# Kernel tuning notes

Measured on AMD Instinct MI355X. Metric: run time of the kernel, lower is better.

Reference implementation:

```python
import jax, jax.numpy as jnp
import numpy as np
import math

B, L, D = 8, 2048, 256


def setup_inputs() -> dict:
    key = jax.random.key(0)
    ks = jax.random.split(key, 8)
    return {
        "query": jax.random.normal(ks[0], (B, L, D), dtype=jnp.float32),
        "key": jax.random.normal(ks[1], (B, L, D), dtype=jnp.float32),
        "value": jax.random.normal(ks[2], (B, L, D), dtype=jnp.float32),
        "mask": jax.random.randint(ks[3], (B, L), 0, 2, dtype=jnp.int32),
        "Wq_w": jax.random.normal(ks[4], (D, D), dtype=jnp.float32) * 0.05,
        "Wq_b": jax.random.normal(ks[5], (D,), dtype=jnp.float32) * 0.05,
        "Wk_w": jax.random.normal(ks[6], (D, D), dtype=jnp.float32) * 0.05,
        "Wk_b": jax.random.normal(ks[7], (D,), dtype=jnp.float32) * 0.05,
    }


def reference(query, key, value, mask, Wq_w, Wq_b, Wk_w, Wk_b):
    d = query.shape[-1]
    q = query @ Wq_w.T + Wq_b            # [B, Lq, D]
    k = key @ Wk_w.T + Wk_b              # [B, Lk, D]
    scores = jnp.einsum("bqd,bkd->bqk", q, k) / math.sqrt(d)  # [B, Lq, Lk]
    m = mask.astype(scores.dtype)[:, None, :]                  # [B, 1, Lk]
    # multiplicative then additive masking, as in original
    scores = jnp.where(m == 0, jnp.asarray(-1e9, scores.dtype), scores * m)
    attn = jax.nn.softmax(scores, axis=-1)
    return jnp.einsum("bqk,bkd->bqd", attn, value)
```

## Files before the change

### kernel.cpp

```cpp
#include <hip/hip_runtime.h>
#include <stdint.h>
#include <stddef.h>

#define B_ 8
#define L_ 2048
#define D_ 256
#define KSPLIT 4
#define KRANGE 512
#define KTILE 32
#define NITER 16
#define PSS 40

typedef __bf16 bf16x8 __attribute__((ext_vector_type(8)));
typedef float floatx4 __attribute__((ext_vector_type(4)));
typedef _Float16 half4_t __attribute__((ext_vector_type(4)));

__device__ __forceinline__ short f2bf(float f) {
    union { float f; uint32_t u; } v; v.f = f;
    return (short)((v.u + 0x8000u) >> 16);
}

__device__ __forceinline__ uint32_t pack2bf(float a, float b) {
    union { float f; uint32_t u; } x, y; x.f = a; y.f = b;
    return ((x.u + 0x8000u) >> 16) | ((y.u + 0x8000u) & 0xFFFF0000u);
}

__device__ __forceinline__ void async16(const void* g, void* l) {
    __builtin_amdgcn_global_load_lds(
        (__attribute__((address_space(1))) void*)g,
        (__attribute__((address_space(3))) void*)l,
        16, 0, 0);
}

__global__ __launch_bounds__(256, 3) void proj_kernel(
    const float* __restrict__ Xq, const float* __restrict__ Xk,
    const float* __restrict__ Wq, const float* __restrict__ Wk,
    const float* __restrict__ bq, const float* __restrict__ bk,
    short* __restrict__ Oq, short* __restrict__ Ok)
{
    const float* X    = blockIdx.y ? Xk : Xq;
    const float* W    = blockIdx.y ? Wk : Wq;
    const float* bias = blockIdx.y ? bk : bq;
    short* Out        = blockIdx.y ? Ok : Oq;

    __shared__ uint32_t As[2][64 * 20];
    __shared__ uint32_t Ws[2][256 * 20];

    const int tid  = threadIdx.x;
    const int wid  = tid >> 6;
    const int lane = tid & 63;
    const int m16  = lane & 15;
    const int quad = lane >> 4;
    const int row0 = blockIdx.x * 64;
    const int ar = tid >> 2, cg = tid & 3;

    floatx4 acc[16];
    const floatx4 z4 = {0.f, 0.f, 0.f, 0.f};
#pragma unroll
    for (int i = 0; i < 16; i++) acc[i] = z4;

    {
        const float* srcA = X + (size_t)(row0 + ar) * D_ + cg * 8;
        float4 a = *(const float4*)srcA, b2 = *(const float4*)(srcA + 4);
        uint4 u; u.x = pack2bf(a.x, a.y); u.y = pack2bf(a.z, a.w);
        u.z = pack2bf(b2.x, b2.y); u.w = pack2bf(b2.z, b2.w);
        *(uint4*)&As[0][ar * 20 + cg * 4] = u;
#pragma unroll
        for (int p = 0; p < 4; p++) {
            const float* srcW = W + (size_t)(p * 64 + ar) * D_ + cg * 8;
            float4 wa = *(const float4*)srcW, wb = *(const float4*)(srcW + 4);
            uint4 w; w.x = pack2bf(wa.x, wa.y); w.y = pack2bf(wa.z, wa.w);
            w.z = pack2bf(wb.x, wb.y); w.w = pack2bf(wb.z, wb.w);
            *(uint4*)&Ws[0][(p * 64 + ar) * 20 + cg * 4] = w;
        }
    }
    __syncthreads();

    for (int kc = 0; kc < 8; kc++) {
        const int buf = kc & 1;
        float4 na, nb, nwa[4], nwb[4];
        if (kc < 7) {
            const int k1 = (kc + 1) * 32;
            const float* srcA = X + (size_t)(row0 + ar) * D_ + k1 + cg * 8;
            na = *(const float4*)srcA; nb = *(const float4*)(srcA + 4);
#pragma unroll
            for (int p = 0; p < 4; p++) {
                const float* srcW = W + (size_t)(p * 64 + ar) * D_ + k1 + cg * 8;
                nwa[p] = *(const float4*)srcW; nwb[p] = *(const float4*)(srcW + 4);
            }
        }
        bf16x8 af = *(const bf16x8*)&As[buf][(wid * 16 + m16) * 20 + quad * 4];
#pragma unroll
        for (int n = 0; n < 16; n++) {
            bf16x8 bfr = *(const bf16x8*)&Ws[buf][(n * 16 + m16) * 20 + quad * 4];
            acc[n] = __builtin_amdgcn_mfma_f32_16x16x32_bf16(af, bfr, acc[n], 0, 0, 0);
        }
        if (kc < 7) {
            uint4 u; u.x = pack2bf(na.x, na.y); u.y = pack2bf(na.z, na.w);
            u.z = pack2bf(nb.x, nb.y); u.w = pack2bf(nb.z, nb.w);
            *(uint4*)&As[buf ^ 1][ar * 20 + cg * 4] = u;
#pragma unroll
            for (int p = 0; p < 4; p++) {
                uint4 w; w.x = pack2bf(nwa[p].x, nwa[p].y); w.y = pack2bf(nwa[p].z, nwa[p].w);
                w.z = pack2bf(nwb[p].x, nwb[p].y); w.w = pack2bf(nwb[p].z, nwb[p].w);
                *(uint4*)&Ws[buf ^ 1][(p * 64 + ar) * 20 + cg * 4] = w;
            }
        }
        __syncthreads();
    }
#pragma unroll
    for (int n = 0; n < 16; n++) {
        const int col = n * 16 + m16;
        const float bv = bias[col];
#pragma unroll
        for (int r = 0; r < 4; r++) {
            const int row = row0 + wid * 16 + quad * 4 + r;
            Out[(size_t)row * D_ + col] = f2bf(acc[n][r] + bv);
        }
    }
}

__global__ __launch_bounds__(256, 2) void vtrans_kernel(
    const float* __restrict__ V, short* __restrict__ Vt)
{
    __shared__ uint32_t T[256 * 20];
    const int tid = threadIdx.x;
    const int b  = blockIdx.y;
    const int l0 = blockIdx.x * 32;
    const int r2 = tid >> 4;
    const int dg = tid & 15;
    const int lp = r2 ^ ((dg & 3) << 2);
#pragma unroll
    for (int p = 0; p < 4; p++) {
        int d0 = (dg + p * 16) * 4;
        const float* src = V + ((size_t)b * L_ + l0 + r2 * 2) * D_ + d0;
        float4 e0 = *(const float4*)src;
        float4 e1 = *(const float4*)(src + D_);
        T[(d0 + 0) * 20 + lp] = pack2bf(e0.x, e1.x);
        T[(d0 + 1) * 20 + lp] = pack2bf(e0.y, e1.y);
        T[(d0 + 2) * 20 + lp] = pack2bf(e0.z, e1.z);
        T[(d0 + 3) * 20 + lp] = pack2bf(e0.w, e1.w);
    }
    __syncthreads();
#pragma unroll
    for (int p = 0; p < 4; p++) {
        int d = (tid >> 2) + p * 64;
        int c = tid & 3;
        int cp = c ^ ((d >> 2) & 3);
        uint4 u = *(const uint4*)&T[d * 20 + cp * 4];
        *(uint4*)(Vt + ((size_t)b * D_ + d) * L_ + l0 + c * 8) = u;
    }
}

__global__ __launch_bounds__(256, 2) void flash_kernel(
    const short* __restrict__ Qb, const short* __restrict__ Kb,
    const short* __restrict__ Vt, const int* __restrict__ mask,
    float* __restrict__ Out, _Float16* __restrict__ Part,
    float* __restrict__ Lpart)
{
    __shared__ short Ks[2][KTILE * 256];
    __shared__ short Vs[2][256 * KTILE];
    __shared__ short Ps[4 * 32 * PSS];

    const int tid  = threadIdx.x;
    const int wid  = tid >> 6;
    const int lane = tid & 63;
    const int m16  = lane & 15;
    const int quad = lane >> 4;
    const int b  = blockIdx.x;
    const int q0 = blockIdx.y * 128;
    const int z  = blockIdx.z;

    const short* kbase = Kb + ((size_t)b * L_ + z * KRANGE) * D_;
    const short* vbase = Vt + (size_t)b * D_ * L_;
    const int*   mg    = mask + b * L_ + z * KRANGE;

    bf16x8 qf[2][8];
    {
        const short* qrow = Qb + ((size_t)b * L_ + q0 + wid * 32) * D_;
#pragma unroll
        for (int s2 = 0; s2 < 2; s2++)
#pragma unroll
            for (int kk = 0; kk < 8; kk++)
                qf[s2][kk] = *(const bf16x8*)(qrow + (size_t)(s2 * 16 + m16) * D_ + kk * 32 + quad * 8);
    }

    floatx4 o[2][16];
    const floatx4 z4 = {0.f, 0.f, 0.f, 0.f};
#pragma unroll
    for (int s2 = 0; s2 < 2; s2++)
#pragma unroll
        for (int n = 0; n < 16; n++) o[s2][n] = z4;
    float rsum[2][4] = {{0.f,0.f,0.f,0.f},{0.f,0.f,0.f,0.f}};

    auto stageK = [&](int t, int bufi) {
        short* kl = &Ks[bufi][0];
#pragma unroll
        for (int c = 0; c < 4; c++) {
            int unit = wid * 4 + c;
            int row = unit * 2 + (lane >> 5);
            int g = (lane & 31) ^ (row & 7);
            async16(kbase + (size_t)(t * KTILE + row) * D_ + g * 8, kl + unit * 512);
        }
    };
    auto stageV = [&](int t, int bufi) {
        short* vl = &Vs[bufi][0];
#pragma unroll
        for (int c = 0; c < 4; c++) {
            int unit = wid * 4 + c;
            int d = unit * 16 + (lane >> 2);
            int g = (lane & 3) ^ ((lane >> 2) & 3);
            async16(vbase + (size_t)d * L_ + z * KRANGE + t * KTILE + g * 8, vl + unit * 512);
        }
    };

    stageK(0, 0);
    __builtin_amdgcn_s_waitcnt(0x0F70);
    __syncthreads();

    short* ps = Ps + wid * (32 * PSS);
    const float C2 = 0.09016844f;
    bf16x8 pf0, pf1;

    for (int t = 0; t < NITER; t++) {
        const int buf = t & 1;
        if (t + 1 < NITER) stageK(t + 1, buf ^ 1);
        stageV(t, buf);
        const short* kl = &Ks[buf][0];

        int mv0 = mg[t * KTILE + m16];
        int mv1 = mg[t * KTILE + 16 + m16];

        floatx4 sA[2][2];
#pragma unroll
        for (int s2 = 0; s2 < 2; s2++) { sA[s2][0] = z4; sA[s2][1] = z4; }
#pragma unroll
        for (int kk = 0; kk < 8; kk++) {
#pragma unroll
            for (int j = 0; j < 2; j++) {
                int row = j * 16 + m16;
                int cidx = (kk * 4 + quad) ^ (m16 & 7);
                bf16x8 kf = *(const bf16x8*)(kl + row * 256 + cidx * 8);
                sA[0][j] = __builtin_amdgcn_mfma_f32_16x16x32_bf16(qf[0][kk], kf, sA[0][j], 0, 0, 0);
                sA[1][j] = __builtin_amdgcn_mfma_f32_16x16x32_bf16(qf[1][kk], kf, sA[1][j], 0, 0, 0);
            }
        }

        if (t > 0) {
            const short* vl = &Vs[buf ^ 1][0];
#pragma unroll
            for (int n = 0; n < 16; n++) {
                int rowd = n * 16 + m16;
                int cidx = quad ^ (m16 & 3);
                bf16x8 vf = *(const bf16x8*)(vl + rowd * 32 + cidx * 8);
                o[0][n] = __builtin_amdgcn_mfma_f32_16x16x32_bf16(pf0, vf, o[0][n], 0, 0, 0);
                o[1][n] = __builtin_amdgcn_mfma_f32_16x16x32_bf16(pf1, vf, o[1][n], 0, 0, 0);
            }
        }

        float moff0 = mv0 ? 0.f : -1.0e30f;
        float moff1 = mv1 ? 0.f : -1.0e30f;
#pragma unroll
        for (int s2 = 0; s2 < 2; s2++) {
#pragma unroll
            for (int j = 0; j < 2; j++) {
                const float moff = j ? moff1 : moff0;
#pragma unroll
                for (int r = 0; r < 4; r++) {
                    float p = exp2f(fmaf(sA[s2][j][r], C2, moff));
                    rsum[s2][r] += p;
                    ps[(s2 * 16 + quad * 4 + r) * PSS + j * 16 + m16] = f2bf(p);
                }
            }
        }
        __builtin_amdgcn_s_waitcnt(0xC07F);
        pf0 = *(const bf16x8*)(ps + (size_t)m16 * PSS + quad * 8);
        pf1 = *(const bf16x8*)(ps + (size_t)(16 + m16) * PSS + quad * 8);

        __builtin_amdgcn_s_waitcnt(0x0F70);
        __syncthreads();
    }

    {
        const short* vl = &Vs[(NITER - 1) & 1][0];
#pragma unroll
        for (int n = 0; n < 16; n++) {
            int rowd = n * 16 + m16;
            int cidx = quad ^ (m16 & 3);
            bf16x8 vf = *(const bf16x8*)(vl + rowd * 32 + cidx * 8);
            o[0][n] = __builtin_amdgcn_mfma_f32_16x16x32_bf16(pf0, vf, o[0][n], 0, 0, 0);
            o[1][n] = __builtin_amdgcn_mfma_f32_16x16x32_bf16(pf1, vf, o[1][n], 0, 0, 0);
        }
    }

#pragma unroll
    for (int s2 = 0; s2 < 2; s2++)
#pragma unroll
        for (int r = 0; r < 4; r++) {
            float x = rsum[s2][r];
            x += __shfl_xor(x, 1, 16);
            x += __shfl_xor(x, 2, 16);
            x += __shfl_xor(x, 4, 16);
            x += __shfl_xor(x, 8, 16);
            rsum[s2][r] = x;
        }

    const size_t BLD = (size_t)B_ * L_ * D_;
    const size_t rowbase = (size_t)b * L_ + q0 + wid * 32;
    if (z == 0) {
        float* po = Out + rowbase * D_;
#pragma unroll
        for (int s2 = 0; s2 < 2; s2++)
#pragma unroll
            for (int n = 0; n < 16; n++)
#pragma unroll
                for (int r = 0; r < 4; r++)
                    po[(size_t)(s2 * 16 + quad * 4 + r) * D_ + n * 16 + m16] = o[s2][n][r];
    } else {
        _Float16* pp = Part + (size_t)(z - 1) * BLD + rowbase * D_;
#pragma unroll
        for (int s2 = 0; s2 < 2; s2++)
#pragma unroll
            for (int n = 0; n < 16; n++)
#pragma unroll
                for (int r = 0; r < 4; r++)
                    pp[(size_t)(s2 * 16 + quad * 4 + r) * D_ + n * 16 + m16] = (_Float16)o[s2][n][r];
    }
    if (m16 == 0) {
#pragma unroll
        for (int s2 = 0; s2 < 2; s2++)
#pragma unroll
            for (int r = 0; r < 4; r++)
                Lpart[(size_t)z * (B_ * L_) + rowbase + s2 * 16 + quad * 4 + r] = rsum[s2][r];
    }
}

__global__ __launch_bounds__(256) void norm_kernel(
    float* __restrict__ Out, const _Float16* __restrict__ Part,
    const float* __restrict__ Lpart)
{
    const int idx = blockIdx.x * 256 + threadIdx.x;
    const int row = idx >> 6;
    const int c   = (idx & 63) * 4;
    const size_t off = (size_t)row * D_ + c;
    const size_t BLD = (size_t)B_ * L_ * D_;
    float4 acc = *(float4*)(Out + off);
#pragma unroll
    for (int zz = 0; zz < 3; zz++) {
        half4_t h = *(const half4_t*)(Part + zz * BLD + off);
        acc.x += (float)h.x; acc.y += (float)h.y;
        acc.z += (float)h.z; acc.w += (float)h.w;
    }
    const int BL = B_ * L_;
    float l = Lpart[row] + Lpart[BL + row] + Lpart[2 * BL + row] + Lpart[3 * BL + row];
    float inv = 1.0f / l;
    acc.x *= inv; acc.y *= inv; acc.z *= inv; acc.w *= inv;
    *(float4*)(Out + off) = acc;
}

extern "C" void kernel_launch(void* const* d_in, const int* in_sizes, int n_in,
                              void* d_out, int out_size, void* d_ws, size_t ws_size,
                              hipStream_t stream) {
    const float* query = (const float*)d_in[0];
    const float* key   = (const float*)d_in[1];
    const float* value = (const float*)d_in[2];
    const int*   mask  = (const int*)d_in[3];
    const float* Wq_w  = (const float*)d_in[4];
    const float* Wq_b  = (const float*)d_in[5];
    const float* Wk_w  = (const float*)d_in[6];
    const float* Wk_b  = (const float*)d_in[7];
    float* out = (float*)d_out;

    const size_t BLD = (size_t)B_ * L_ * D_;
    short* qb = (short*)d_ws;
    short* kb = qb + BLD;
    short* vt = kb + BLD;
    _Float16* part = (_Float16*)(vt + BLD);
    float* lpart = (float*)(part + 3 * BLD);

    proj_kernel<<<dim3(256, 2), 256, 0, stream>>>(query, key, Wq_w, Wk_w, Wq_b, Wk_b, qb, kb);
    vtrans_kernel<<<dim3(64, 8), 256, 0, stream>>>(value, vt);
    flash_kernel<<<dim3(8, 16, 4), 256, 0, stream>>>(qb, kb, vt, mask, out, part, lpart);
    norm_kernel<<<dim3((B_ * L_ * D_ / 4) / 256), 256, 0, stream>>>(out, part, lpart);
}
```

Measured before the change: 189.6 us.

## Switch flash kernel to 32x32x16 MFMA with register-resident P via permlane swap

Recasts both attention GEMMs from 16x16x32 to 32x32x16 bf16 MFMA, computing S transposed (K as A operand) so each lane holds one query column. The softmax probabilities are packed to bf16 with v_cvt_pk_bf16_f32 and shuffled into the PV operand layout using v_permlane32_swap, removing the LDS round-trip for P and its buffer. Masking becomes a ballot bitmask selecting exp or zero, the row-sum reduction becomes a single shuffle, and s_setprio raises priority around MFMA blocks. The new layout relies on correct lane/register mapping for the permlane swap and output stores.

```diff
diff --git a/kernel.cpp b/kernel.cpp
--- a/kernel.cpp
+++ b/kernel.cpp
@@ -9,10 +9,10 @@
 #define KRANGE 512
 #define KTILE 32
 #define NITER 16
-#define PSS 40
 
 typedef __bf16 bf16x8 __attribute__((ext_vector_type(8)));
 typedef float floatx4 __attribute__((ext_vector_type(4)));
+typedef float floatx16 __attribute__((ext_vector_type(16)));
 typedef _Float16 half4_t __attribute__((ext_vector_type(4)));
 
 __device__ __forceinline__ short f2bf(float f) {
@@ -23,6 +23,16 @@
 __device__ __forceinline__ uint32_t pack2bf(float a, float b) {
     union { float f; uint32_t u; } x, y; x.f = a; y.f = b;
     return ((x.u + 0x8000u) >> 16) | ((y.u + 0x8000u) & 0xFFFF0000u);
+}
+
+__device__ __forceinline__ uint32_t cvtpk_bf16(float lo, float hi2) {
+    uint32_t w;
+    asm("v_cvt_pk_bf16_f32 %0, %1, %2" : "=v"(w) : "v"(lo), "v"(hi2));
+    return w;
+}
+
+__device__ __forceinline__ void pl32swap(uint32_t &a, uint32_t &b) {
+    asm("v_permlane32_swap_b32 %0, %1" : "+v"(a), "+v"(b));
 }
 
 __device__ __forceinline__ void async16(const void* g, void* l) {
@@ -160,13 +170,12 @@
 {
     __shared__ short Ks[2][KTILE * 256];
     __shared__ short Vs[2][256 * KTILE];
-    __shared__ short Ps[4 * 32 * PSS];
 
     const int tid  = threadIdx.x;
     const int wid  = tid >> 6;
     const int lane = tid & 63;
-    const int m16  = lane & 15;
-    const int quad = lane >> 4;
+    const int l31  = lane & 31;
+    const int hi   = lane >> 5;
     const int b  = blockIdx.x;
     const int q0 = blockIdx.y * 128;
     const int z  = blockIdx.z;
@@ -175,23 +184,20 @@
     const short* vbase = Vt + (size_t)b * D_ * L_;
     const int*   mg    = mask + b * L_ + z * KRANGE;
 
-    bf16x8 qf[2][8];
+    bf16x8 qf[16];
     {
-        const short* qrow = Qb + ((size_t)b * L_ + q0 + wid * 32) * D_;
-#pragma unroll
-        for (int s2 = 0; s2 < 2; s2++)
-#pragma unroll
-            for (int kk = 0; kk < 8; kk++)
-                qf[s2][kk] = *(const bf16x8*)(qrow + (size_t)(s2 * 16 + m16) * D_ + kk * 32 + quad * 8);
-    }
-
-    floatx4 o[2][16];
-    const floatx4 z4 = {0.f, 0.f, 0.f, 0.f};
-#pragma unroll
-    for (int s2 = 0; s2 < 2; s2++)
-#pragma unroll
-        for (int n = 0; n < 16; n++) o[s2][n] = z4;
-    float rsum[2][4] = {{0.f,0.f,0.f,0.f},{0.f,0.f,0.f,0.f}};
+        const short* qrow = Qb + ((size_t)b * L_ + q0 + wid * 32 + l31) * D_ + hi * 8;
+#pragma unroll
+        for (int dt = 0; dt < 16; dt++)
+            qf[dt] = *(const bf16x8*)(qrow + dt * 16);
+    }
+
+    floatx16 o[8];
+#pragma unroll
+    for (int n = 0; n < 8; n++)
+#pragma unroll
+        for (int r = 0; r < 16; r++) o[n][r] = 0.f;
+    float rsum = 0.f;
 
     auto stageK = [&](int t, int bufi) {
         short* kl = &Ks[bufi][0];
@@ -218,9 +224,8 @@
     __builtin_amdgcn_s_waitcnt(0x0F70);
     __syncthreads();
 
-    short* ps = Ps + wid * (32 * PSS);
     const float C2 = 0.09016844f;
-    bf16x8 pf0, pf1;
+    bf16x8 pfA, pfB;
 
     for (int t = 0; t < NITER; t++) {
         const int buf = t & 1;
@@ -228,54 +233,55 @@
         stageV(t, buf);
         const short* kl = &Ks[buf][0];
 
-        int mv0 = mg[t * KTILE + m16];
-        int mv1 = mg[t * KTILE + 16 + m16];
-
-        floatx4 sA[2][2];
-#pragma unroll
-        for (int s2 = 0; s2 < 2; s2++) { sA[s2][0] = z4; sA[s2][1] = z4; }
-#pragma unroll
-        for (int kk = 0; kk < 8; kk++) {
-#pragma unroll
-            for (int j = 0; j < 2; j++) {
-                int row = j * 16 + m16;
-                int cidx = (kk * 4 + quad) ^ (m16 & 7);
-                bf16x8 kf = *(const bf16x8*)(kl + row * 256 + cidx * 8);
-                sA[0][j] = __builtin_amdgcn_mfma_f32_16x16x32_bf16(qf[0][kk], kf, sA[0][j], 0, 0, 0);
-                sA[1][j] = __builtin_amdgcn_mfma_f32_16x16x32_bf16(qf[1][kk], kf, sA[1][j], 0, 0, 0);
-            }
-        }
+        int mv = mg[t * KTILE + l31];
+
+        floatx16 s;
+#pragma unroll
+        for (int r = 0; r < 16; r++) s[r] = 0.f;
+        __builtin_amdgcn_s_setprio(1);
+#pragma unroll
+        for (int dt = 0; dt < 16; dt++) {
+            int g = (dt * 2 + hi) ^ (l31 & 7);
+            bf16x8 kf = *(const bf16x8*)(kl + l31 * 256 + g * 8);
+            s = __builtin_amdgcn_mfma_f32_32x32x16_bf16(kf, qf[dt], s, 0, 0, 0);
+        }
+        __builtin_amdgcn_s_setprio(0);
 
         if (t > 0) {
             const short* vl = &Vs[buf ^ 1][0];
-#pragma unroll
-            for (int n = 0; n < 16; n++) {
-                int rowd = n * 16 + m16;
-                int cidx = quad ^ (m16 & 3);
-                bf16x8 vf = *(const bf16x8*)(vl + rowd * 32 + cidx * 8);
-                o[0][n] = __builtin_amdgcn_mfma_f32_16x16x32_bf16(pf0, vf, o[0][n], 0, 0, 0);
-                o[1][n] = __builtin_amdgcn_mfma_f32_16x16x32_bf16(pf1, vf, o[1][n], 0, 0, 0);
-            }
-        }
-
-        float moff0 = mv0 ? 0.f : -1.0e30f;
-        float moff1 = mv1 ? 0.f : -1.0e30f;
-#pragma unroll
-        for (int s2 = 0; s2 < 2; s2++) {
-#pragma unroll
-            for (int j = 0; j < 2; j++) {
-                const float moff = j ? moff1 : moff0;
-#pragma unroll
-                for (int r = 0; r < 4; r++) {
-                    float p = exp2f(fmaf(sA[s2][j][r], C2, moff));
-                    rsum[s2][r] += p;
-                    ps[(s2 * 16 + quad * 4 + r) * PSS + j * 16 + m16] = f2bf(p);
+            __builtin_amdgcn_s_setprio(1);
+#pragma unroll
+            for (int n = 0; n < 8; n++) {
+                int d = n * 32 + l31;
+#pragma unroll
+                for (int kh = 0; kh < 2; kh++) {
+                    int g2 = (kh * 2 + hi) ^ (l31 & 3);
+                    bf16x8 vf = *(const bf16x8*)(vl + d * 32 + g2 * 8);
+                    o[n] = __builtin_amdgcn_mfma_f32_32x32x16_bf16(kh ? pfB : pfA, vf, o[n], 0, 0, 0);
                 }
             }
-        }
-        __builtin_amdgcn_s_waitcnt(0xC07F);
-        pf0 = *(const bf16x8*)(ps + (size_t)m16 * PSS + quad * 8);
-        pf1 = *(const bf16x8*)(ps + (size_t)(16 + m16) * PSS + quad * 8);
+            __builtin_amdgcn_s_setprio(0);
+        }
+
+        uint32_t mb = (uint32_t)__ballot(mv != 0) >> (hi * 4);
+        uint32_t w[8];
+#pragma unroll
+        for (int i = 0; i < 8; i++) {
+            const int r0 = 2 * i, r1 = 2 * i + 1;
+            const int k0 = (r0 & 3) + 8 * (r0 >> 2);
+            float e0 = ((mb >> k0) & 1) ? exp2f(s[r0] * C2) : 0.f;
+            float e1 = ((mb >> (k0 + 1)) & 1) ? exp2f(s[r1] * C2) : 0.f;
+            rsum += e0 + e1;
+            w[i] = cvtpk_bf16(e0, e1);
+        }
+        pl32swap(w[0], w[2]); pl32swap(w[1], w[3]);
+        pl32swap(w[4], w[6]); pl32swap(w[5], w[7]);
+        {
+            union { uint32_t u[4]; bf16x8 v; } ua, ub;
+            ua.u[0] = w[0]; ua.u[1] = w[1]; ua.u[2] = w[2]; ua.u[3] = w[3];
+            ub.u[0] = w[4]; ub.u[1] = w[5]; ub.u[2] = w[6]; ub.u[3] = w[7];
+            pfA = ua.v; pfB = ub.v;
+        }
 
         __builtin_amdgcn_s_waitcnt(0x0F70);
         __syncthreads();
@@ -283,55 +289,45 @@
 
     {
         const short* vl = &Vs[(NITER - 1) & 1][0];
-#pragma unroll
-        for (int n = 0; n < 16; n++) {
-            int rowd = n * 16 + m16;
-            int cidx = quad ^ (m16 & 3);
-            bf16x8 vf = *(const bf16x8*)(vl + rowd * 32 + cidx * 8);
-            o[0][n] = __builtin_amdgcn_mfma_f32_16x16x32_bf16(pf0, vf, o[0][n], 0, 0, 0);
-            o[1][n] = __builtin_amdgcn_mfma_f32_16x16x32_bf16(pf1, vf, o[1][n], 0, 0, 0);
-        }
-    }
-
-#pragma unroll
-    for (int s2 = 0; s2 < 2; s2++)
-#pragma unroll
-        for (int r = 0; r < 4; r++) {
-            float x = rsum[s2][r];
-            x += __shfl_xor(x, 1, 16);
-            x += __shfl_xor(x, 2, 16);
-            x += __shfl_xor(x, 4, 16);
-            x += __shfl_xor(x, 8, 16);
-            rsum[s2][r] = x;
-        }
+        __builtin_amdgcn_s_setprio(1);
+#pragma unroll
+        for (int n = 0; n < 8; n++) {
+            int d = n * 32 + l31;
+#pragma unroll
+            for (int kh = 0; kh < 2; kh++) {
+                int g2 = (kh * 2 + hi) ^ (l31 & 3);
+                bf16x8 vf = *(const bf16x8*)(vl + d * 32 + g2 * 8);
+                o[n] = __builtin_amdgcn_mfma_f32_32x32x16_bf16(kh ? pfB : pfA, vf, o[n], 0, 0, 0);
+            }
+        }
+        __builtin_amdgcn_s_setprio(0);
+    }
+
+    rsum += __shfl_xor(rsum, 32);
 
     const size_t BLD = (size_t)B_ * L_ * D_;
     const size_t rowbase = (size_t)b * L_ + q0 + wid * 32;
     if (z == 0) {
         float* po = Out + rowbase * D_;
 #pragma unroll
-        for (int s2 = 0; s2 < 2; s2++)
-#pragma unroll
-            for (int n = 0; n < 16; n++)
-#pragma unroll
-                for (int r = 0; r < 4; r++)
-                    po[(size_t)(s2 * 16 + quad * 4 + r) * D_ + n * 16 + m16] = o[s2][n][r];
+        for (int n = 0; n < 8; n++)
+#pragma unroll
+            for (int r = 0; r < 16; r++) {
+                int q = (r & 3) + 8 * (r >> 2) + 4 * hi;
+                po[(size_t)q * D_ + n * 32 + l31] = o[n][r];
+            }
     } else {
         _Float16* pp = Part + (size_t)(z - 1) * BLD + rowbase * D_;
 #pragma unroll
-        for (int s2 = 0; s2 < 2; s2++)
-#pragma unroll
-            for (int n = 0; n < 16; n++)
-#pragma unroll
-                for (int r = 0; r < 4; r++)
-                    pp[(size_t)(s2 * 16 + quad * 4 + r) * D_ + n * 16 + m16] = (_Float16)o[s2][n][r];
-    }
-    if (m16 == 0) {
-#pragma unroll
-        for (int s2 = 0; s2 < 2; s2++)
-#pragma unroll
-            for (int r = 0; r < 4; r++)
-                Lpart[(size_t)z * (B_ * L_) + rowbase + s2 * 16 + quad * 4 + r] = rsum[s2][r];
+        for (int n = 0; n < 8; n++)
+#pragma unroll
+            for (int r = 0; r < 16; r++) {
+                int q = (r & 3) + 8 * (r >> 2) + 4 * hi;
+                pp[(size_t)q * D_ + n * 32 + l31] = (_Float16)o[n][r];
+            }
+    }
+    if (lane < 32) {
+        Lpart[(size_t)z * (B_ * L_) + rowbase + lane] = rsum;
     }
 }
 
```

After: 185.7 us. -2.1%, faster.
